# Kernel tuning notes

Hardware: AMD Instinct MI355X
Metric: run time of the kernel (lower is better)

The kernel has to match this reference:

```python
import jax, jax.numpy as jnp
import numpy as np

B, T, D, H, C = 256, 512, 128, 512, 10

def setup_inputs() -> dict:
    key = jax.random.key(0)
    ks = jax.random.split(key, 12)
    s_x = 1.0 / np.sqrt(D)
    s_h = 1.0 / np.sqrt(H)
    inp = {
        'x':   jax.random.normal(ks[0], (B, T, D), dtype=jnp.float32),
        'wgx': jax.random.normal(ks[1], (D, H), dtype=jnp.float32) * s_x,
        'wgh': jax.random.normal(ks[2], (H, H), dtype=jnp.float32) * s_h,
        'bg':  jnp.zeros((H,), dtype=jnp.float32),
        'wix': jax.random.normal(ks[3], (D, H), dtype=jnp.float32) * s_x,
        'wih': jax.random.normal(ks[4], (H, H), dtype=jnp.float32) * s_h,
        'bi':  jnp.zeros((H,), dtype=jnp.float32),
        'wfx': jax.random.normal(ks[5], (D, H), dtype=jnp.float32) * s_x,
        'wfh': jax.random.normal(ks[6], (H, H), dtype=jnp.float32) * s_h,
        'bf':  jnp.ones((H,), dtype=jnp.float32),  # forget bias = 1 as in source
        'wox': jax.random.normal(ks[7], (D, H), dtype=jnp.float32) * s_x,
        'woh': jax.random.normal(ks[8], (H, H), dtype=jnp.float32) * s_h,
        'bo':  jnp.zeros((H,), dtype=jnp.float32),
        'wph': jax.random.normal(ks[9], (H, C), dtype=jnp.float32) * s_h,
        'bp':  jnp.zeros((C,), dtype=jnp.float32),
    }
    return inp

def reference(x, wgx, wgh, bg, wix, wih, bi, wfx, wfh, bf, wox, woh, bo, wph, bp):
    # Precompute all input projections as one big batched GEMM per gate: [B,T,H]
    xg = jnp.einsum('btd,dh->bth', x, wgx) + bg
    xi = jnp.einsum('btd,dh->bth', x, wix) + bi
    xf = jnp.einsum('btd,dh->bth', x, wfx) + bf
    xo = jnp.einsum('btd,dh->bth', x, wox) + bo

    def step(carry, xt):
        h_prev, c_prev = carry
        xg_t, xi_t, xf_t, xo_t = xt
        gt = jnp.tanh(xg_t + h_prev @ wgh)
        it = jax.nn.sigmoid(xi_t + h_prev @ wih)
        ft = jax.nn.sigmoid(xf_t + h_prev @ wfh)
        ot = jax.nn.sigmoid(xo_t + h_prev @ woh)
        ct = gt * it + c_prev * ft
        ht = jnp.tanh(ct) * ot
        return (ht, ct), None

    h0 = jnp.zeros((x.shape[0], wgh.shape[0]), dtype=x.dtype)
    c0 = jnp.zeros_like(h0)
    # scan over time: move T to leading axis
    xs = (xg.swapaxes(0, 1), xi.swapaxes(0, 1), xf.swapaxes(0, 1), xo.swapaxes(0, 1))
    (hT, _), _ = jax.lax.scan(step, (h0, c0), xs)
    return hT @ wph + bp
```

## Files before the change

kernel.cpp:

```cpp
#include <hip/hip_runtime.h>
#include <hip/hip_bf16.h>
#include <stdint.h>

typedef __attribute__((ext_vector_type(8))) short short8;
typedef __attribute__((ext_vector_type(4))) float floatx4;
typedef __attribute__((ext_vector_type(4))) int intx4;
typedef __attribute__((ext_vector_type(2))) unsigned long long ull2;
typedef __attribute__((ext_vector_type(4))) unsigned short ushort4v;

#define DEVI __device__ __forceinline__

constexpr int B_ = 256, T_ = 512, D_ = 128, H_ = 512, C_ = 10;
constexpr int KTOT = H_ + D_;
constexpr int RG = 16;
constexpr int NBG = 16;
constexpr int NCG = 16;
constexpr int HCW = 32;

constexpr size_t OFF_XB = 0;
constexpr size_t SZ_XB  = (size_t)B_ * T_ * D_ * 2;
constexpr size_t OFF_WC = OFF_XB + SZ_XB;
constexpr size_t SZ_WC  = (size_t)4 * H_ * KTOT * 2;
constexpr size_t OFF_HB = OFF_WC + SZ_WC;
constexpr size_t SZ_HB  = (size_t)2 * B_ * H_ * 2;
constexpr size_t OFF_CT = OFF_HB + SZ_HB;
constexpr size_t SZ_CT  = (size_t)NBG * (T_ + 1) * 4;
constexpr size_t WS_NEED = OFF_CT + SZ_CT;

DEVI uint16_t f2bf(float f) {
    uint32_t u = __builtin_bit_cast(uint32_t, f);
    u += 0x7FFFu + ((u >> 16) & 1u);
    return (uint16_t)(u >> 16);
}
DEVI float bf2f(uint16_t u) {
    return __builtin_bit_cast(float, (uint32_t)u << 16);
}
DEVI float sigf(float x)  { return 1.0f / (1.0f + __expf(-x)); }
DEVI float tanhf_(float x){ return 1.0f - 2.0f / (1.0f + __expf(2.0f * x)); }

__global__ void k_cvt_x(const float* __restrict__ x, uint16_t* __restrict__ xb) {
    int i = (blockIdx.x * 256 + threadIdx.x) * 4;
    float4 v = *reinterpret_cast<const float4*>(x + i);
    ushort4v o;
    o.x = f2bf(v.x); o.y = f2bf(v.y); o.z = f2bf(v.z); o.w = f2bf(v.w);
    *reinterpret_cast<ushort4v*>(xb + i) = o;
}

__global__ void k_build_w(const float* __restrict__ wgh, const float* __restrict__ wih,
                          const float* __restrict__ wfh, const float* __restrict__ woh,
                          const float* __restrict__ wgx, const float* __restrict__ wix,
                          const float* __restrict__ wfx, const float* __restrict__ wox,
                          uint16_t* __restrict__ wc) {
    int np = blockIdx.x;
    int g = np >> 9, n = np & 511;
    const float* wh = (g == 0) ? wgh : (g == 1) ? wih : (g == 2) ? wfh : woh;
    const float* wx = (g == 0) ? wgx : (g == 1) ? wix : (g == 2) ? wfx : wox;
    for (int k = threadIdx.x; k < KTOT; k += 256) {
        float v = (k < H_) ? wh[(size_t)k * H_ + n] : wx[(size_t)(k - H_) * H_ + n];
        wc[(size_t)np * KTOT + k] = f2bf(v);
    }
}

__global__ __launch_bounds__(256, 1) void k_lstm(
    const uint16_t* __restrict__ xb,
    const uint16_t* __restrict__ wc,
    const float* __restrict__ bgp, const float* __restrict__ bip,
    const float* __restrict__ bfp, const float* __restrict__ bop,
    uint16_t* hbuf,
    int* counters)
{
    __shared__ __align__(16) short hx[RG * KTOT];
    __shared__ float pre[4][RG][HCW + 1];

    const int tid  = threadIdx.x;
    const int lane = tid & 63;
    const int w    = tid >> 6;
    const int bid  = blockIdx.x;
    const int xcd = bid & 7, j = bid >> 3;
    const int bg = xcd * 2 + (j >> 4);
    const int cg = j & 15;
    const int b0  = bg * RG;
    const int hc0 = cg * HCW;

    short8 bfr[2][20];
    {
        const int lcol = lane & 15, kgrp = lane >> 4;
        #pragma unroll
        for (int t2 = 0; t2 < 2; ++t2) {
            const uint16_t* src = wc + (size_t)(w * H_ + hc0 + t2 * 16 + lcol) * KTOT + kgrp * 8;
            #pragma unroll
            for (int ks = 0; ks < 20; ++ks)
                bfr[t2][ks] = *reinterpret_cast<const short8*>(src + ks * 32);
        }
    }

    const int erow = tid >> 4;
    const int ep   = tid & 15;
    const int hcg0 = hc0 + ep * 2;
    float bge[2], bie[2], bfe[2], boe[2], cst[2] = {0.f, 0.f};
    #pragma unroll
    for (int e = 0; e < 2; ++e) {
        bge[e] = bgp[hcg0 + e]; bie[e] = bip[hcg0 + e];
        bfe[e] = bfp[hcg0 + e]; boe[e] = bop[hcg0 + e];
    }

    const int srow = tid >> 4, sseg = tid & 15;
    const int sswz = (srow & 7) << 4;
    const int arow = lane & 15, akg = lane >> 4;
    const int abase = arow * (KTOT * 2) + akg * 16;
    const int aswz  = (arow & 7) << 4;

    int* ctr = counters + bg * (T_ + 1);
    char* lds = (char*)hx;

    for (int t = 0; t < T_; ++t) {
        {
            const short8 xv = *reinterpret_cast<const short8*>(
                xb + ((size_t)(b0 + srow) * T_ + t) * D_ + sseg * 8);
            int byte = srow * (KTOT * 2) + H_ * 2 + sseg * 16;
            *reinterpret_cast<short8*>(lds + (byte ^ sswz)) = xv;
        }

        if (t > 0) {
            if (tid == 0) {
                int it = 0;
                while (__hip_atomic_load(ctr + t, __ATOMIC_RELAXED, __HIP_MEMORY_SCOPE_AGENT) < NCG) {
                    if (++it > (1 << 28)) break;
                    __builtin_amdgcn_s_sleep(1);
                }
                asm volatile("" ::: "memory");
            }
            __syncthreads();
        }

        if (t == 0) {
            intx4 z = {0, 0, 0, 0};
            #pragma unroll
            for (int c4 = 0; c4 < 4; ++c4) {
                int byte = srow * (KTOT * 2) + sseg * 64 + c4 * 16;
                *reinterpret_cast<intx4*>(lds + (byte ^ sswz)) = z;
            }
        } else {
            const unsigned long long* src = reinterpret_cast<const unsigned long long*>(
                hbuf + (size_t)(t & 1) * B_ * H_ + (size_t)(b0 + srow) * H_ + sseg * 32);
            #pragma unroll
            for (int c4 = 0; c4 < 4; ++c4) {
                unsigned long long lo = __hip_atomic_load(src + c4 * 2,     __ATOMIC_RELAXED, __HIP_MEMORY_SCOPE_AGENT);
                unsigned long long hi = __hip_atomic_load(src + c4 * 2 + 1, __ATOMIC_RELAXED, __HIP_MEMORY_SCOPE_AGENT);
                ull2 v; v.x = lo; v.y = hi;
                int byte = srow * (KTOT * 2) + sseg * 64 + c4 * 16;
                *reinterpret_cast<ull2*>(lds + (byte ^ sswz)) = v;
            }
        }
        __syncthreads();

        floatx4 acc0 = {0.f, 0.f, 0.f, 0.f}, acc1 = {0.f, 0.f, 0.f, 0.f};
        #pragma unroll
        for (int ks = 0; ks < 20; ++ks) {
            int byte = (abase + ks * 64) ^ aswz;
            short8 a = *reinterpret_cast<const short8*>(lds + byte);
            acc0 = __builtin_amdgcn_mfma_f32_16x16x32_bf16(a, bfr[0][ks], acc0, 0, 0, 0);
            acc1 = __builtin_amdgcn_mfma_f32_16x16x32_bf16(a, bfr[1][ks], acc1, 0, 0, 0);
        }
        #pragma unroll
        for (int r = 0; r < 4; ++r) {
            pre[w][(lane >> 4) * 4 + r][(lane & 15)]      = acc0[r];
            pre[w][(lane >> 4) * 4 + r][16 + (lane & 15)] = acc1[r];
        }
        __syncthreads();

        float hp[2];
        #pragma unroll
        for (int e = 0; e < 2; ++e) {
            int col = ep * 2 + e;
            float ag = pre[0][erow][col] + bge[e];
            float ai = pre[1][erow][col] + bie[e];
            float af = pre[2][erow][col] + bfe[e];
            float ao = pre[3][erow][col] + boe[e];
            float g = tanhf_(ag), ii = sigf(ai), f = sigf(af), o = sigf(ao);
            float c = g * ii + cst[e] * f;
            cst[e] = c;
            hp[e] = tanhf_(c) * o;
        }
        uint32_t packed = (uint32_t)f2bf(hp[0]) | ((uint32_t)f2bf(hp[1]) << 16);
        uint32_t* hdst = reinterpret_cast<uint32_t*>(
            hbuf + (size_t)((t + 1) & 1) * B_ * H_ + (size_t)(b0 + erow) * H_ + hcg0);
        __hip_atomic_store(hdst, packed, __ATOMIC_RELAXED, __HIP_MEMORY_SCOPE_AGENT);
        asm volatile("s_waitcnt vmcnt(0)" ::: "memory");
        __syncthreads();
        if (tid == 0)
            __hip_atomic_fetch_add(ctr + t + 1, 1, __ATOMIC_RELAXED, __HIP_MEMORY_SCOPE_AGENT);
    }
}

__global__ void k_proj(const uint16_t* __restrict__ hb0, const float* __restrict__ wph,
                       const float* __restrict__ bp, float* __restrict__ out) {
    int b = blockIdx.x, lane = threadIdx.x;
    const uint32_t* hrow = reinterpret_cast<const uint32_t*>(hb0 + (size_t)b * H_);
    float p[C_];
    #pragma unroll
    for (int c = 0; c < C_; ++c) p[c] = 0.f;
    #pragma unroll
    for (int q = 0; q < 4; ++q) {
        int k2 = lane + q * 64;
        uint32_t u = __hip_atomic_load(hrow + k2, __ATOMIC_RELAXED, __HIP_MEMORY_SCOPE_AGENT);
        float h0 = bf2f((uint16_t)(u & 0xFFFFu));
        float h1 = bf2f((uint16_t)(u >> 16));
        #pragma unroll
        for (int c = 0; c < C_; ++c)
            p[c] += h0 * wph[(size_t)(2 * k2) * C_ + c] + h1 * wph[(size_t)(2 * k2 + 1) * C_ + c];
    }
    #pragma unroll
    for (int c = 0; c < C_; ++c) {
        float v = p[c];
        #pragma unroll
        for (int off = 32; off; off >>= 1) v += __shfl_down(v, off, 64);
        if (lane == 0) out[(size_t)b * C_ + c] = v + bp[c];
    }
}

extern "C" void kernel_launch(void* const* d_in, const int* in_sizes, int n_in,
                              void* d_out, int out_size, void* d_ws, size_t ws_size,
                              hipStream_t stream) {
    const float* x   = (const float*)d_in[0];
    const float* wgx = (const float*)d_in[1];
    const float* wgh = (const float*)d_in[2];
    const float* bg  = (const float*)d_in[3];
    const float* wix = (const float*)d_in[4];
    const float* wih = (const float*)d_in[5];
    const float* bi  = (const float*)d_in[6];
    const float* wfx = (const float*)d_in[7];
    const float* wfh = (const float*)d_in[8];
    const float* bf  = (const float*)d_in[9];
    const float* wox = (const float*)d_in[10];
    const float* woh = (const float*)d_in[11];
    const float* bo  = (const float*)d_in[12];
    const float* wph = (const float*)d_in[13];
    const float* bp  = (const float*)d_in[14];

    if (ws_size < WS_NEED) return;

    char* ws = (char*)d_ws;
    uint16_t* xbp = (uint16_t*)(ws + OFF_XB);
    uint16_t* wcp = (uint16_t*)(ws + OFF_WC);
    uint16_t* hbp = (uint16_t*)(ws + OFF_HB);
    int*      ctp = (int*)(ws + OFF_CT);

    hipMemsetAsync(ctp, 0, SZ_CT, stream);
    k_cvt_x<<<(B_ * T_ * D_) / (256 * 4), 256, 0, stream>>>(x, xbp);
    k_build_w<<<4 * H_, 256, 0, stream>>>(wgh, wih, wfh, woh, wgx, wix, wfx, wox, wcp);
    k_lstm<<<256, 256, 0, stream>>>(xbp, wcp, bg, bi, bf, bo, hbp, ctp);
    k_proj<<<B_, 64, 0, stream>>>(hbp , wph, bp, (float*)d_out);
}
```

Measured before the change: 1.604 ms.

## Interleave gate columns per wave so the cell update runs in registers via shuffles

Each wave now loads weight columns for all four gates of the same 8 hidden units (g/i in one MFMA tile, f/o in the other), instead of one gate per wave. The cell update then pulls the partner gate with an xor-8 lane shuffle rather than staging pre-activations through shared memory. This removes the LDS write/read and one __syncthreads per timestep on the serial critical path. In exchange, half the lanes compute redundantly, and the h stores become 16-bit atomic stores, four per lane, instead of packed 32-bit ones.

```diff
diff --git a/kernel.cpp b/kernel.cpp
--- a/kernel.cpp
+++ b/kernel.cpp
@@ -70,7 +70,6 @@
     int* counters)
 {
     __shared__ __align__(16) short hx[RG * KTOT];
-    __shared__ float pre[4][RG][HCW + 1];
 
     const int tid  = threadIdx.x;
     const int lane = tid & 63;
@@ -82,33 +81,37 @@
     const int b0  = bg * RG;
     const int hc0 = cg * HCW;
 
-    short8 bfr[2][20];
+    short8 bf0[20], bf1[20];
     {
         const int lcol = lane & 15, kgrp = lane >> 4;
-        #pragma unroll
-        for (int t2 = 0; t2 < 2; ++t2) {
-            const uint16_t* src = wc + (size_t)(w * H_ + hc0 + t2 * 16 + lcol) * KTOT + kgrp * 8;
-            #pragma unroll
-            for (int ks = 0; ks < 20; ++ks)
-                bfr[t2][ks] = *reinterpret_cast<const short8*>(src + ks * 32);
-        }
-    }
-
-    const int erow = tid >> 4;
-    const int ep   = tid & 15;
-    const int hcg0 = hc0 + ep * 2;
-    float bge[2], bie[2], bfe[2], boe[2], cst[2] = {0.f, 0.f};
-    #pragma unroll
-    for (int e = 0; e < 2; ++e) {
-        bge[e] = bgp[hcg0 + e]; bie[e] = bip[hcg0 + e];
-        bfe[e] = bfp[hcg0 + e]; boe[e] = bop[hcg0 + e];
-    }
+        const int cl = lcol & 7, hi = lcol >> 3;
+        const int colg = hc0 + w * 8 + cl;
+        const size_t row0 = (size_t)((0 + hi) * H_ + colg) * KTOT;
+        const size_t row1 = (size_t)((2 + hi) * H_ + colg) * KTOT;
+        #pragma unroll
+        for (int ks = 0; ks < 20; ++ks) {
+            bf0[ks] = *reinterpret_cast<const short8*>(wc + row0 + kgrp * 8 + ks * 32);
+            bf1[ks] = *reinterpret_cast<const short8*>(wc + row1 + kgrp * 8 + ks * 32);
+        }
+        #pragma unroll
+        for (int ks = 0; ks < 20; ++ks) {
+            asm volatile("" : "+v"(bf0[ks]));
+            asm volatile("" : "+v"(bf1[ks]));
+        }
+    }
+
+    const int cl   = lane & 7;
+    const int mycol = hc0 + w * 8 + cl;
+    const bool lo  = (lane & 8) == 0;
+    const float bgv = bgp[mycol], biv = bip[mycol], bfv = bfp[mycol], bov = bop[mycol];
+    float cst[4] = {0.f, 0.f, 0.f, 0.f};
 
     const int srow = tid >> 4, sseg = tid & 15;
     const int sswz = (srow & 7) << 4;
     const int arow = lane & 15, akg = lane >> 4;
     const int abase = arow * (KTOT * 2) + akg * 16;
     const int aswz  = (arow & 7) << 4;
+    const int hrow0 = (lane >> 4) * 4;
 
     int* ctr = counters + bg * (T_ + 1);
     char* lds = (char*)hx;
@@ -145,9 +148,9 @@
                 hbuf + (size_t)(t & 1) * B_ * H_ + (size_t)(b0 + srow) * H_ + sseg * 32);
             #pragma unroll
             for (int c4 = 0; c4 < 4; ++c4) {
-                unsigned long long lo = __hip_atomic_load(src + c4 * 2,     __ATOMIC_RELAXED, __HIP_MEMORY_SCOPE_AGENT);
-                unsigned long long hi = __hip_atomic_load(src + c4 * 2 + 1, __ATOMIC_RELAXED, __HIP_MEMORY_SCOPE_AGENT);
-                ull2 v; v.x = lo; v.y = hi;
+                unsigned long long lov = __hip_atomic_load(src + c4 * 2,     __ATOMIC_RELAXED, __HIP_MEMORY_SCOPE_AGENT);
+                unsigned long long hiv = __hip_atomic_load(src + c4 * 2 + 1, __ATOMIC_RELAXED, __HIP_MEMORY_SCOPE_AGENT);
+                ull2 v; v.x = lov; v.y = hiv;
                 int byte = srow * (KTOT * 2) + sseg * 64 + c4 * 16;
                 *reinterpret_cast<ull2*>(lds + (byte ^ sswz)) = v;
             }
@@ -159,33 +162,31 @@
         for (int ks = 0; ks < 20; ++ks) {
             int byte = (abase + ks * 64) ^ aswz;
             short8 a = *reinterpret_cast<const short8*>(lds + byte);
-            acc0 = __builtin_amdgcn_mfma_f32_16x16x32_bf16(a, bfr[0][ks], acc0, 0, 0, 0);
-            acc1 = __builtin_amdgcn_mfma_f32_16x16x32_bf16(a, bfr[1][ks], acc1, 0, 0, 0);
-        }
+            acc0 = __builtin_amdgcn_mfma_f32_16x16x32_bf16(a, bf0[ks], acc0, 0, 0, 0);
+            acc1 = __builtin_amdgcn_mfma_f32_16x16x32_bf16(a, bf1[ks], acc1, 0, 0, 0);
+        }
+
+        uint16_t hp[4];
         #pragma unroll
         for (int r = 0; r < 4; ++r) {
-            pre[w][(lane >> 4) * 4 + r][(lane & 15)]      = acc0[r];
-            pre[w][(lane >> 4) * 4 + r][16 + (lane & 15)] = acc1[r];
-        }
-        __syncthreads();
-
-        float hp[2];
-        #pragma unroll
-        for (int e = 0; e < 2; ++e) {
-            int col = ep * 2 + e;
-            float ag = pre[0][erow][col] + bge[e];
-            float ai = pre[1][erow][col] + bie[e];
-            float af = pre[2][erow][col] + bfe[e];
-            float ao = pre[3][erow][col] + boe[e];
+            float p0 = acc0[r], p1 = acc1[r];
+            float q0 = __shfl_xor(p0, 8, 64);
+            float q1 = __shfl_xor(p1, 8, 64);
+            float ag = (lo ? p0 : q0) + bgv;
+            float ai = (lo ? q0 : p0) + biv;
+            float af = (lo ? p1 : q1) + bfv;
+            float ao = (lo ? q1 : p1) + bov;
             float g = tanhf_(ag), ii = sigf(ai), f = sigf(af), o = sigf(ao);
-            float c = g * ii + cst[e] * f;
-            cst[e] = c;
-            hp[e] = tanhf_(c) * o;
-        }
-        uint32_t packed = (uint32_t)f2bf(hp[0]) | ((uint32_t)f2bf(hp[1]) << 16);
-        uint32_t* hdst = reinterpret_cast<uint32_t*>(
-            hbuf + (size_t)((t + 1) & 1) * B_ * H_ + (size_t)(b0 + erow) * H_ + hcg0);
-        __hip_atomic_store(hdst, packed, __ATOMIC_RELAXED, __HIP_MEMORY_SCOPE_AGENT);
+            float c = g * ii + cst[r] * f;
+            cst[r] = c;
+            hp[r] = f2bf(tanhf_(c) * o);
+        }
+        if (lo) {
+            uint16_t* hdst = hbuf + (size_t)((t + 1) & 1) * B_ * H_ + (size_t)(b0 + hrow0) * H_ + mycol;
+            #pragma unroll
+            for (int r = 0; r < 4; ++r)
+                __hip_atomic_store(hdst + (size_t)r * H_, hp[r], __ATOMIC_RELAXED, __HIP_MEMORY_SCOPE_AGENT);
+        }
         asm volatile("s_waitcnt vmcnt(0)" ::: "memory");
         __syncthreads();
         if (tid == 0)
```

After: 1.806 ms. 1.13x slower.
